# Optimization experiments

Hardware: AMD Instinct MI355X
Metric: run time of the kernel (lower is better)

The kernel has to match this reference:

```python
import jax, jax.numpy as jnp
import numpy as np

B, C_IN, C_OUT, K, L = 8, 512, 512, 5, 4096
RED = 128  # max(int(512*0.25), 4)
STRIDE, PAD, DIL, GROUPS = 1, 2, 1, 1


def setup_inputs() -> dict:
    key = jax.random.key(0)
    ks = jax.random.split(key, 20)

    def n(k, shape, scale=0.05):
        return jax.random.normal(k, shape, jnp.float32) * scale

    inp = {
        "x": jax.random.normal(ks[0], (B, C_IN, L), jnp.float32),
        "weight": n(ks[1], (C_OUT, C_IN // GROUPS, K), 0.05),
        "bias": jnp.zeros((C_OUT,), jnp.float32),
    }
    # four attention branches: avgpool -> 1x1 conv (C_in->RED) -> relu -> 1x1 conv (RED->out) -> sigmoid
    for i, (nm, od) in enumerate(zip(["ka", "sa", "ia", "oa"], [K, 1, C_IN, C_OUT])):
        inp[nm + "_w1"] = n(ks[2 + 4 * i], (RED, C_IN))
        inp[nm + "_b1"] = jnp.zeros((RED,), jnp.float32)
        inp[nm + "_w2"] = n(ks[3 + 4 * i], (od, RED))
        inp[nm + "_b2"] = jnp.zeros((od,), jnp.float32)
    return inp


def _att(avg, w1, b1, w2, b2):
    # avg: [B, C_in]; two 1x1 convs over a length-1 signal == two dense layers
    h = jax.nn.relu(avg @ w1.T + b1)
    return jax.nn.sigmoid(h @ w2.T + b2)


def reference(x, weight, bias,
              ka_w1, ka_b1, ka_w2, ka_b2,
              sa_w1, sa_b1, sa_w2, sa_b2,
              ia_w1, ia_b1, ia_w2, ia_b2,
              oa_w1, oa_b1, oa_w2, oa_b2):
    b, c, l = x.shape
    avg = x.mean(axis=2)                     # AdaptiveAvgPool1d(1) -> [B, C_in]
    ka = _att(avg, ka_w1, ka_b1, ka_w2, ka_b2)  # [B, K]
    sa = _att(avg, sa_w1, sa_b1, sa_w2, sa_b2)  # [B, 1]
    ia = _att(avg, ia_w1, ia_b1, ia_w2, ia_b2)  # [B, C_in]
    oa = _att(avg, oa_w1, oa_b1, oa_w2, oa_b2)  # [B, C_out]
    # dynamic weight [B, C_out, C_in//g, K]; note ia broadcasts on the OUT-channel
    # axis (faithful to the torch broadcasting, which requires C_in == C_out)
    dw = (weight[None]
          * ka[:, None, None, :]
          * sa[:, :, None, None]
          * ia[:, :, None, None]
          * oa[:, :, None, None])
    dw = dw.reshape(b * C_OUT, C_IN // GROUPS, K)
    xg = x.reshape(1, b * c, l)
    out = jax.lax.conv_general_dilated(
        xg, dw,
        window_strides=(STRIDE,),
        padding=[(PAD, PAD)],
        rhs_dilation=(DIL,),
        feature_group_count=b * GROUPS,
        dimension_numbers=("NCH", "OIH", "NCH"))
    out = out.reshape(b, C_OUT, -1) + bias[None, :, None]
    return out
```

## Files before the change

### kernel.cpp

```cpp
#include <hip/hip_runtime.h>

typedef unsigned short u16;
typedef __bf16 bf16x8 __attribute__((ext_vector_type(8)));
typedef float f32x4 __attribute__((ext_vector_type(4)));
typedef u16 u16x8 __attribute__((ext_vector_type(8)));

#define B_    8
#define CIN   512
#define COUT  512
#define KT    5
#define LEN   4096
#define RED_  128
#define KDIM  (KT * CIN)
#define XTROWS (LEN + 4)
#define NLT   64

__device__ __forceinline__ u16 f2bf(float f) {
    unsigned int u = __float_as_uint(f);
    u += 0x7fffu + ((u >> 16) & 1u);
    return (u16)(u >> 16);
}

typedef __attribute__((address_space(1))) void gvoid_t;
typedef __attribute__((address_space(3))) void lvoid_t;
__device__ __forceinline__ void glds16(const u16* g, u16* l) {
    __builtin_amdgcn_global_load_lds((gvoid_t*)g, (lvoid_t*)l, 16, 0, 0);
}

__global__ __launch_bounds__(256) void xtavg_kernel(const float* __restrict__ x,
                                                    u16* __restrict__ xt,
                                                    float* __restrict__ P) {
    __shared__ __align__(16) unsigned Tu[64 * 65];
    __shared__ float Fp[64 * 2 * 17];
    const int b  = blockIdx.z;
    const int l0 = blockIdx.x * 64;
    const int c0 = blockIdx.y * 128;
    const int tid = threadIdx.x;
    const int lq  = tid & 15;
    const int cpg = tid >> 4;

#pragma unroll
    for (int p = 0; p < 4; ++p) {
        const int cp = p * 16 + cpg;
        const int c  = c0 + cp * 2;
        const float* xa = x + ((size_t)b * CIN + c) * LEN + l0 + lq * 4;
        float4 va = *(const float4*)xa;
        float4 vb = *(const float4*)(xa + LEN);
        unsigned u0 = __builtin_amdgcn_perm(__float_as_uint(vb.x), __float_as_uint(va.x), 0x07060302);
        unsigned u1 = __builtin_amdgcn_perm(__float_as_uint(vb.y), __float_as_uint(va.y), 0x07060302);
        unsigned u2 = __builtin_amdgcn_perm(__float_as_uint(vb.z), __float_as_uint(va.z), 0x07060302);
        unsigned u3 = __builtin_amdgcn_perm(__float_as_uint(vb.w), __float_as_uint(va.w), 0x07060302);
        Tu[(lq * 4 + 0) * 65 + cp] = u0;
        Tu[(lq * 4 + 1) * 65 + cp] = u1;
        Tu[(lq * 4 + 2) * 65 + cp] = u2;
        Tu[(lq * 4 + 3) * 65 + cp] = u3;
        Fp[(cp * 2 + 0) * 17 + lq] = va.x + va.y + va.z + va.w;
        Fp[(cp * 2 + 1) * 17 + lq] = vb.x + vb.y + vb.z + vb.w;
    }
    __syncthreads();

#pragma unroll
    for (int p = 0; p < 4; ++p) {
        const int r  = p * 16 + (tid >> 4);
        const int j4 = (tid & 15) * 4;
        unsigned w0 = Tu[r * 65 + j4 + 0];
        unsigned w1 = Tu[r * 65 + j4 + 1];
        unsigned w2 = Tu[r * 65 + j4 + 2];
        unsigned w3 = Tu[r * 65 + j4 + 3];
        *(uint4*)(xt + ((size_t)b * XTROWS + l0 + 2 + r) * CIN + c0 + j4 * 2) =
            make_uint4(w0, w1, w2, w3);
    }
    if (tid < 128) {
        const float* fp = &Fp[tid * 17];
        float s = 0.f;
#pragma unroll
        for (int k = 0; k < 16; ++k) s += fp[k];
        P[(size_t)blockIdx.x * (B_ * CIN) + b * CIN + c0 + tid] = s;
    }
    if (blockIdx.y == 0 && blockIdx.x == 0 && tid < 128)
        *(uint4*)(xt + ((size_t)b * XTROWS + (tid >> 6)) * CIN + (tid & 63) * 8) =
            make_uint4(0, 0, 0, 0);
    if (blockIdx.y == 0 && blockIdx.x == (LEN / 64 - 1) && tid < 128)
        *(uint4*)(xt + ((size_t)b * XTROWS + LEN + 2 + (tid >> 6)) * CIN + (tid & 63) * 8) =
            make_uint4(0, 0, 0, 0);
}

__global__ void attn_kernel(const float* __restrict__ P,
    const float* kw1, const float* kb1, const float* kw2, const float* kb2,
    const float* sw1, const float* sb1, const float* sw2, const float* sb2,
    const float* iw1, const float* ib1, const float* iw2, const float* ib2,
    const float* ow1, const float* ob1, const float* ow2, const float* ob2,
    float* __restrict__ ka, float* __restrict__ sa,
    float* __restrict__ ia, float* __restrict__ oa) {
    const int br = blockIdx.x >> 3, b = blockIdx.x & 7;
    const float *w1, *b1p, *w2, *b2p; float* op; int od;
    if (br == 0)      { w1 = kw1; b1p = kb1; w2 = kw2; b2p = kb2; op = ka + b * KT;  od = KT;   }
    else if (br == 1) { w1 = sw1; b1p = sb1; w2 = sw2; b2p = sb2; op = sa + b;       od = 1;    }
    else if (br == 2) { w1 = iw1; b1p = ib1; w2 = iw2; b2p = ib2; op = ia + b * CIN; od = CIN;  }
    else              { w1 = ow1; b1p = ob1; w2 = ow2; b2p = ob2; op = oa + b * COUT; od = COUT; }

    __shared__ float av[4 * 132];
    __shared__ float h[RED_];
    const int t = threadIdx.x;
    {
        const float* pp = P + b * CIN + t;
        float ssum = 0.f;
#pragma unroll 8
        for (int lt = 0; lt < NLT; ++lt) ssum += pp[(size_t)lt * (B_ * CIN)];
        av[(t >> 7) * 132 + (t & 127)] = ssum * (1.0f / LEN);
    }
    __syncthreads();

    const int row = t >> 2, part = t & 3;
    float acc = 0.f;
    const float4* wr = (const float4*)(w1 + (size_t)row * CIN + part * 128);
    const float* ap = &av[part * 132];
#pragma unroll 8
    for (int c = 0; c < 32; ++c) {
        float4 w = wr[c];
        acc += ap[4 * c] * w.x + ap[4 * c + 1] * w.y + ap[4 * c + 2] * w.z + ap[4 * c + 3] * w.w;
    }
    acc += __shfl_down(acc, 1, 64);
    acc += __shfl_down(acc, 2, 64);
    if (part == 0) h[row] = fmaxf(acc + b1p[row], 0.f);
    __syncthreads();

    for (int o = t; o < od; o += 512) {
        float a2 = b2p[o];
        const float4* w2r = (const float4*)(w2 + (size_t)o * RED_);
#pragma unroll 8
        for (int j = 0; j < RED_ / 4; ++j) {
            float4 w = w2r[j];
            a2 += h[4 * j] * w.x + h[4 * j + 1] * w.y + h[4 * j + 2] * w.z + h[4 * j + 3] * w.w;
        }
        op[o] = 1.f / (1.f + expf(-a2));
    }
}

__global__ void wbgen_kernel(const float* __restrict__ w, const float* __restrict__ ka,
                             u16* __restrict__ wb) {
    __shared__ float kv[B_ * KT];
    const int tid = threadIdx.x;
    if (tid < B_ * KT) kv[tid] = ka[tid];
    __syncthreads();
    const int o  = (blockIdx.x >> 2) * 4 + (tid >> 6);
    const int b0 = (blockIdx.x & 3) * 2;
    const int i8 = (tid & 63) * 8;

    const float* wp = w + ((size_t)o * CIN + i8) * KT;
    float wv[40];
#pragma unroll
    for (int q = 0; q < 10; ++q) {
        float4 v = ((const float4*)wp)[q];
        wv[4 * q] = v.x; wv[4 * q + 1] = v.y; wv[4 * q + 2] = v.z; wv[4 * q + 3] = v.w;
    }
#pragma unroll
    for (int bb = 0; bb < 2; ++bb) {
        const int b = b0 + bb;
#pragma unroll
        for (int k = 0; k < KT; ++k) {
            const float s = kv[b * KT + k];
            u16x8 r;
#pragma unroll
            for (int j = 0; j < 8; ++j) r[j] = f2bf(wv[j * KT + k] * s);
            *(u16x8*)(wb + ((size_t)(b * COUT + o)) * KDIM + k * CIN + i8) = r;
        }
    }
}

__global__ __launch_bounds__(256, 2) void gemm_kernel(
    const u16* __restrict__ wb, const u16* __restrict__ xt,
    const float* __restrict__ sa, const float* __restrict__ ia,
    const float* __restrict__ oa, const float* __restrict__ bias,
    float* __restrict__ out) {
    __shared__ __align__(16) u16 As[5 * 128 * 32];
    __shared__ __align__(16) u16 Bs[260 * 32];
    __shared__ float sm[128], bm[128];

    const int orig = blockIdx.x;
    const int wg   = (orig & 7) * 64 + (orig >> 3);
    const int l0 = (wg & 15) * 256;
    const int o0 = ((wg >> 4) & 3) * 128;
    const int b  = wg >> 6;
    const int tid = threadIdx.x;

    if (tid < 128) {
        sm[tid] = sa[b] * ia[b * CIN + o0 + tid] * oa[b * COUT + o0 + tid];
        bm[tid] = bias[o0 + tid];
    }

    const int lane = tid & 63;
    const int wave = tid >> 6;
    const int wm = (wave >> 1) * 64;
    const int wn = (wave & 1) * 128;
    const int lm = lane & 15;
    const int quad = lane >> 4;

    f32x4 acc[4][8];
#pragma unroll
    for (int i = 0; i < 4; ++i)
#pragma unroll
        for (int j = 0; j < 8; ++j) {
            f32x4 zz = {0.f, 0.f, 0.f, 0.f};
            acc[i][j] = zz;
        }

    const u16* gA = wb + ((size_t)(b * COUT + o0 + (tid >> 2))) * KDIM + (tid & 3) * 8;
    const u16* gB = xt + ((size_t)b * XTROWS + l0) * CIN;

#pragma unroll 1
    for (int ic = 0; ic < 16; ++ic) {
        const int i0 = ic * 32;
#pragma unroll
        for (int t = 0; t < KT; ++t) {
            glds16(gA + t * 512 + i0, &As[t * 4096 + tid * 8]);
            glds16(gA + (size_t)64 * KDIM + t * 512 + i0, &As[t * 4096 + 2048 + tid * 8]);
        }
#pragma unroll
        for (int r = 0; r < 4; ++r) {
            const int slot = r * 256 + tid;
            glds16(gB + (size_t)(slot >> 2) * CIN + i0 + (slot & 3) * 8, &Bs[slot * 8]);
        }
        if (tid < 16)
            glds16(gB + (size_t)(256 + (tid >> 2)) * CIN + i0 + (tid & 3) * 8,
                   &Bs[(1024 + tid) * 8]);
        __syncthreads();

#pragma unroll
        for (int t = 0; t < KT; ++t) {
            bf16x8 af[4], bfr[8];
#pragma unroll
            for (int f = 0; f < 4; ++f)
                af[f] = *(const bf16x8*)&As[t * 4096 + (wm + f * 16 + lm) * 32 + quad * 8];
#pragma unroll
            for (int f = 0; f < 8; ++f)
                bfr[f] = *(const bf16x8*)&Bs[(wn + f * 16 + lm + t) * 32 + quad * 8];
#pragma unroll
            for (int mt = 0; mt < 4; ++mt)
#pragma unroll
                for (int nt = 0; nt < 8; ++nt)
                    acc[mt][nt] = __builtin_amdgcn_mfma_f32_16x16x32_bf16(
                        af[mt], bfr[nt], acc[mt][nt], 0, 0, 0);
        }
        __syncthreads();
    }

#pragma unroll
    for (int mt = 0; mt < 4; ++mt) {
        const int mb = wm + mt * 16 + quad * 4;
        float sv[4], bv[4];
#pragma unroll
        for (int r = 0; r < 4; ++r) { sv[r] = sm[mb + r]; bv[r] = bm[mb + r]; }
#pragma unroll
        for (int nt = 0; nt < 8; ++nt) {
            const int col = l0 + wn + nt * 16 + lm;
            float* op = out + ((size_t)(b * COUT + o0 + mb)) * LEN + col;
#pragma unroll
            for (int r = 0; r < 4; ++r)
                op[(size_t)r * LEN] = sv[r] * acc[mt][nt][r] + bv[r];
        }
    }
}

extern "C" void kernel_launch(void* const* d_in, const int* in_sizes, int n_in,
                              void* d_out, int out_size, void* d_ws, size_t ws_size,
                              hipStream_t stream) {
    const float* x      = (const float*)d_in[0];
    const float* weight = (const float*)d_in[1];
    const float* bias   = (const float*)d_in[2];
    float* out = (float*)d_out;

    char* ws = (char*)d_ws;
    size_t off = 0;
    auto alloc = [&](size_t bytes) {
        void* p = ws + off;
        off += (bytes + 255) & ~(size_t)255;
        return p;
    };
    u16*   wbuf = (u16*)alloc((size_t)B_ * COUT * KDIM * sizeof(u16));
    u16*   xtb  = (u16*)alloc((size_t)B_ * XTROWS * CIN * sizeof(u16));
    float* Pbuf = (float*)alloc((size_t)NLT * B_ * CIN * sizeof(float));
    float* ka   = (float*)alloc((size_t)B_ * KT * sizeof(float));
    float* sa   = (float*)alloc((size_t)B_ * sizeof(float));
    float* ia   = (float*)alloc((size_t)B_ * CIN * sizeof(float));
    float* oa   = (float*)alloc((size_t)B_ * COUT * sizeof(float));

    xtavg_kernel<<<dim3(LEN / 64, CIN / 128, B_), 256, 0, stream>>>(x, xtb, Pbuf);
    attn_kernel<<<32, 512, 0, stream>>>(Pbuf,
        (const float*)d_in[3],  (const float*)d_in[4],  (const float*)d_in[5],  (const float*)d_in[6],
        (const float*)d_in[7],  (const float*)d_in[8],  (const float*)d_in[9],  (const float*)d_in[10],
        (const float*)d_in[11], (const float*)d_in[12], (const float*)d_in[13], (const float*)d_in[14],
        (const float*)d_in[15], (const float*)d_in[16], (const float*)d_in[17], (const float*)d_in[18],
        ka, sa, ia, oa);
    wbgen_kernel<<<(COUT / 4) * 4, 256, 0, stream>>>(weight, ka, wbuf);
    gemm_kernel<<<512, 256, 0, stream>>>(wbuf, xtb, sa, ia, oa, bias, out);
}
```

Before: 241.2 us.

## Fuse attention branches and weight generation into one prep kernel with redundant ka

Merges the attention kernel and the dynamic-weight generation kernel into a single launch. Each of the 1024 weight-gen blocks recomputes the kernel-attention (ka) branch for its batch locally, which removes the dependency on a separate launch. 32 extra blocks are launched and 24 of them compute the sa/ia/oa branches, which are only consumed later by the GEMM. This drops one kernel launch and its serialization gap. In exchange, every weight-gen block redundantly reads the partial sums and the ka weights.

```diff
diff --git a/kernel.cpp b/kernel.cpp
--- a/kernel.cpp
+++ b/kernel.cpp
@@ -85,48 +85,34 @@
             make_uint4(0, 0, 0, 0);
 }
 
-__global__ void attn_kernel(const float* __restrict__ P,
-    const float* kw1, const float* kb1, const float* kw2, const float* kb2,
-    const float* sw1, const float* sb1, const float* sw2, const float* sb2,
-    const float* iw1, const float* ib1, const float* iw2, const float* ib2,
-    const float* ow1, const float* ob1, const float* ow2, const float* ob2,
-    float* __restrict__ ka, float* __restrict__ sa,
-    float* __restrict__ ia, float* __restrict__ oa) {
-    const int br = blockIdx.x >> 3, b = blockIdx.x & 7;
-    const float *w1, *b1p, *w2, *b2p; float* op; int od;
-    if (br == 0)      { w1 = kw1; b1p = kb1; w2 = kw2; b2p = kb2; op = ka + b * KT;  od = KT;   }
-    else if (br == 1) { w1 = sw1; b1p = sb1; w2 = sw2; b2p = sb2; op = sa + b;       od = 1;    }
-    else if (br == 2) { w1 = iw1; b1p = ib1; w2 = iw2; b2p = ib2; op = ia + b * CIN; od = CIN;  }
-    else              { w1 = ow1; b1p = ob1; w2 = ow2; b2p = ob2; op = oa + b * COUT; od = COUT; }
-
-    __shared__ float av[4 * 132];
-    __shared__ float h[RED_];
-    const int t = threadIdx.x;
-    {
-        const float* pp = P + b * CIN + t;
-        float ssum = 0.f;
+__device__ __forceinline__ void attn_branch(
+    int tid, const float* __restrict__ P,
+    const float* w1, const float* b1, const float* w2, const float* b2,
+    float* op, int od, int b, float* av, float* h) {
+#pragma unroll
+    for (int half = 0; half < 2; ++half) {
+        const int ch = tid + half * 256;
+        const float* pp = P + b * CIN + ch;
+        float s = 0.f;
 #pragma unroll 8
-        for (int lt = 0; lt < NLT; ++lt) ssum += pp[(size_t)lt * (B_ * CIN)];
-        av[(t >> 7) * 132 + (t & 127)] = ssum * (1.0f / LEN);
+        for (int lt = 0; lt < NLT; ++lt) s += pp[(size_t)lt * (B_ * CIN)];
+        av[ch] = s * (1.0f / LEN);
     }
     __syncthreads();
-
-    const int row = t >> 2, part = t & 3;
+    const int row = tid >> 1, part = tid & 1;
     float acc = 0.f;
-    const float4* wr = (const float4*)(w1 + (size_t)row * CIN + part * 128);
-    const float* ap = &av[part * 132];
+    const float4* wr = (const float4*)(w1 + (size_t)row * CIN + part * 256);
+    const float* ap = av + part * 256;
 #pragma unroll 8
-    for (int c = 0; c < 32; ++c) {
+    for (int c = 0; c < 64; ++c) {
         float4 w = wr[c];
         acc += ap[4 * c] * w.x + ap[4 * c + 1] * w.y + ap[4 * c + 2] * w.z + ap[4 * c + 3] * w.w;
     }
     acc += __shfl_down(acc, 1, 64);
-    acc += __shfl_down(acc, 2, 64);
-    if (part == 0) h[row] = fmaxf(acc + b1p[row], 0.f);
+    if (part == 0) h[row] = fmaxf(acc + b1[row], 0.f);
     __syncthreads();
-
-    for (int o = t; o < od; o += 512) {
-        float a2 = b2p[o];
+    for (int o = tid; o < od; o += 256) {
+        float a2 = b2[o];
         const float4* w2r = (const float4*)(w2 + (size_t)o * RED_);
 #pragma unroll 8
         for (int j = 0; j < RED_ / 4; ++j) {
@@ -137,34 +123,50 @@
     }
 }
 
-__global__ void wbgen_kernel(const float* __restrict__ w, const float* __restrict__ ka,
-                             u16* __restrict__ wb) {
-    __shared__ float kv[B_ * KT];
+__global__ __launch_bounds__(256) void prep2_kernel(
+    const float* __restrict__ P, const float* __restrict__ weight,
+    const float* kw1, const float* kb1, const float* kw2, const float* kb2,
+    const float* sw1, const float* sb1, const float* sw2, const float* sb2,
+    const float* iw1, const float* ib1, const float* iw2, const float* ib2,
+    const float* ow1, const float* ob1, const float* ow2, const float* ob2,
+    float* __restrict__ sa, float* __restrict__ ia, float* __restrict__ oa,
+    u16* __restrict__ wb) {
+    __shared__ float av[CIN];
+    __shared__ float h[RED_];
+    __shared__ float kv[KT];
     const int tid = threadIdx.x;
-    if (tid < B_ * KT) kv[tid] = ka[tid];
-    __syncthreads();
-    const int o  = (blockIdx.x >> 2) * 4 + (tid >> 6);
-    const int b0 = (blockIdx.x & 3) * 2;
-    const int i8 = (tid & 63) * 8;
-
-    const float* wp = w + ((size_t)o * CIN + i8) * KT;
-    float wv[40];
-#pragma unroll
-    for (int q = 0; q < 10; ++q) {
-        float4 v = ((const float4*)wp)[q];
-        wv[4 * q] = v.x; wv[4 * q + 1] = v.y; wv[4 * q + 2] = v.z; wv[4 * q + 3] = v.w;
-    }
-#pragma unroll
-    for (int bb = 0; bb < 2; ++bb) {
-        const int b = b0 + bb;
+
+    if (blockIdx.x < 1024) {
+        const int og = (int)blockIdx.x >> 3;
+        const int b  = (int)blockIdx.x & 7;
+        attn_branch(tid, P, kw1, kb1, kw2, kb2, kv, KT, b, av, h);
+        __syncthreads();
+        const int o  = og * 4 + (tid >> 6);
+        const int i8 = (tid & 63) * 8;
+        const float* wp = weight + ((size_t)o * CIN + i8) * KT;
+        float wv[40];
+#pragma unroll
+        for (int q = 0; q < 10; ++q) {
+            float4 v = ((const float4*)wp)[q];
+            wv[4 * q] = v.x; wv[4 * q + 1] = v.y; wv[4 * q + 2] = v.z; wv[4 * q + 3] = v.w;
+        }
 #pragma unroll
         for (int k = 0; k < KT; ++k) {
-            const float s = kv[b * KT + k];
+            const float s = kv[k];
             u16x8 r;
 #pragma unroll
             for (int j = 0; j < 8; ++j) r[j] = f2bf(wv[j * KT + k] * s);
             *(u16x8*)(wb + ((size_t)(b * COUT + o)) * KDIM + k * CIN + i8) = r;
         }
+    } else {
+        const int vb = (int)blockIdx.x - 1024;
+        if (vb >= 24) return;
+        const int br = vb >> 3, b = vb & 7;
+        const float *w1, *b1, *w2, *b2; float* op; int od;
+        if (br == 0)      { w1 = sw1; b1 = sb1; w2 = sw2; b2 = sb2; op = sa + b;        od = 1;    }
+        else if (br == 1) { w1 = iw1; b1 = ib1; w2 = iw2; b2 = ib2; op = ia + b * CIN;  od = CIN;  }
+        else              { w1 = ow1; b1 = ob1; w2 = ow2; b2 = ob2; op = oa + b * COUT; od = COUT; }
+        attn_branch(tid, P, w1, b1, w2, b2, op, od, b, av, h);
     }
 }
 
@@ -280,18 +282,16 @@
     u16*   wbuf = (u16*)alloc((size_t)B_ * COUT * KDIM * sizeof(u16));
     u16*   xtb  = (u16*)alloc((size_t)B_ * XTROWS * CIN * sizeof(u16));
     float* Pbuf = (float*)alloc((size_t)NLT * B_ * CIN * sizeof(float));
-    float* ka   = (float*)alloc((size_t)B_ * KT * sizeof(float));
     float* sa   = (float*)alloc((size_t)B_ * sizeof(float));
     float* ia   = (float*)alloc((size_t)B_ * CIN * sizeof(float));
     float* oa   = (float*)alloc((size_t)B_ * COUT * sizeof(float));
 
     xtavg_kernel<<<dim3(LEN / 64, CIN / 128, B_), 256, 0, stream>>>(x, xtb, Pbuf);
-    attn_kernel<<<32, 512, 0, stream>>>(Pbuf,
+    prep2_kernel<<<1056, 256, 0, stream>>>(Pbuf, weight,
         (const float*)d_in[3],  (const float*)d_in[4],  (const float*)d_in[5],  (const float*)d_in[6],
         (const float*)d_in[7],  (const float*)d_in[8],  (const float*)d_in[9],  (const float*)d_in[10],
         (const float*)d_in[11], (const float*)d_in[12], (const float*)d_in[13], (const float*)d_in[14],
         (const float*)d_in[15], (const float*)d_in[16], (const float*)d_in[17], (const float*)d_in[18],
-        ka, sa, ia, oa);
-    wbgen_kernel<<<(COUT / 4) * 4, 256, 0, stream>>>(weight, ka, wbuf);
+        sa, ia, oa, wbuf);
     gemm_kernel<<<512, 256, 0, stream>>>(wbuf, xtb, sa, ia, oa, bias, out);
 }
```

After: 268.9 us. 11.5% more time.

## Double-buffer GEMM LDS tiles and split work across 8 waves per block

Applied to the files above, without the earlier changes.

The GEMM kernel now uses 512 threads with 8 waves, each computing a 64x64 subtile, and double-buffers the A and B LDS tiles. It prefetches the next input-channel chunk via direct global-to-LDS loads while computing the current one, syncing with vmcnt waits and raw barriers. The goal is to hide global load latency behind MFMA work. The trade-offs are doubled LDS use, which limits the kernel to one block per CU, and a lower MFMA-to-LDS-read ratio per wave.

```diff
diff --git a/kernel.cpp b/kernel.cpp
--- a/kernel.cpp
+++ b/kernel.cpp
@@ -168,13 +168,13 @@
     }
 }
 
-__global__ __launch_bounds__(256, 2) void gemm_kernel(
+__global__ __launch_bounds__(512, 2) void gemm_kernel(
     const u16* __restrict__ wb, const u16* __restrict__ xt,
     const float* __restrict__ sa, const float* __restrict__ ia,
     const float* __restrict__ oa, const float* __restrict__ bias,
     float* __restrict__ out) {
-    __shared__ __align__(16) u16 As[5 * 128 * 32];
-    __shared__ __align__(16) u16 Bs[260 * 32];
+    __shared__ __align__(16) u16 As[2][5 * 128 * 32];
+    __shared__ __align__(16) u16 Bs[2][260 * 32];
     __shared__ float sm[128], bm[128];
 
     const int orig = blockIdx.x;
@@ -191,16 +191,16 @@
 
     const int lane = tid & 63;
     const int wave = tid >> 6;
-    const int wm = (wave >> 1) * 64;
-    const int wn = (wave & 1) * 128;
+    const int wm = (wave >> 2) * 64;
+    const int wn = (wave & 3) * 64;
     const int lm = lane & 15;
     const int quad = lane >> 4;
 
-    f32x4 acc[4][8];
+    f32x4 acc[4][4];
 #pragma unroll
     for (int i = 0; i < 4; ++i)
 #pragma unroll
-        for (int j = 0; j < 8; ++j) {
+        for (int j = 0; j < 4; ++j) {
             f32x4 zz = {0.f, 0.f, 0.f, 0.f};
             acc[i][j] = zz;
         }
@@ -208,42 +208,54 @@
     const u16* gA = wb + ((size_t)(b * COUT + o0 + (tid >> 2))) * KDIM + (tid & 3) * 8;
     const u16* gB = xt + ((size_t)b * XTROWS + l0) * CIN;
 
+#define STAGE(B_IDX, IC)                                                            \
+    do {                                                                            \
+        const int i0_ = (IC) * 32;                                                  \
+        _Pragma("unroll")                                                           \
+        for (int t_ = 0; t_ < KT; ++t_)                                             \
+            glds16(gA + t_ * 512 + i0_, &As[B_IDX][t_ * 4096 + tid * 8]);           \
+        _Pragma("unroll")                                                           \
+        for (int r_ = 0; r_ < 2; ++r_) {                                            \
+            const int s_ = r_ * 512 + tid;                                          \
+            glds16(gB + (size_t)(s_ >> 2) * CIN + i0_ + (s_ & 3) * 8,               \
+                   &Bs[B_IDX][s_ * 8]);                                             \
+        }                                                                           \
+        if (tid < 16)                                                               \
+            glds16(gB + (size_t)(256 + (tid >> 2)) * CIN + i0_ + (tid & 3) * 8,     \
+                   &Bs[B_IDX][(1024 + tid) * 8]);                                   \
+    } while (0)
+
+    STAGE(0, 0);
+
 #pragma unroll 1
     for (int ic = 0; ic < 16; ++ic) {
-        const int i0 = ic * 32;
+        const int cur = ic & 1;
+        if (ic < 15) {
+            STAGE(cur ^ 1, ic + 1);
+            asm volatile("s_waitcnt vmcnt(7)" ::: "memory");
+        } else {
+            asm volatile("s_waitcnt vmcnt(0)" ::: "memory");
+        }
+        __builtin_amdgcn_s_barrier();
+
 #pragma unroll
         for (int t = 0; t < KT; ++t) {
-            glds16(gA + t * 512 + i0, &As[t * 4096 + tid * 8]);
-            glds16(gA + (size_t)64 * KDIM + t * 512 + i0, &As[t * 4096 + 2048 + tid * 8]);
-        }
-#pragma unroll
-        for (int r = 0; r < 4; ++r) {
-            const int slot = r * 256 + tid;
-            glds16(gB + (size_t)(slot >> 2) * CIN + i0 + (slot & 3) * 8, &Bs[slot * 8]);
-        }
-        if (tid < 16)
-            glds16(gB + (size_t)(256 + (tid >> 2)) * CIN + i0 + (tid & 3) * 8,
-                   &Bs[(1024 + tid) * 8]);
-        __syncthreads();
-
-#pragma unroll
-        for (int t = 0; t < KT; ++t) {
-            bf16x8 af[4], bfr[8];
-#pragma unroll
-            for (int f = 0; f < 4; ++f)
-                af[f] = *(const bf16x8*)&As[t * 4096 + (wm + f * 16 + lm) * 32 + quad * 8];
-#pragma unroll
-            for (int f = 0; f < 8; ++f)
-                bfr[f] = *(const bf16x8*)&Bs[(wn + f * 16 + lm + t) * 32 + quad * 8];
+            bf16x8 af[4], bfr[4];
+#pragma unroll
+            for (int f = 0; f < 4; ++f) {
+                af[f]  = *(const bf16x8*)&As[cur][t * 4096 + (wm + f * 16 + lm) * 32 + quad * 8];
+                bfr[f] = *(const bf16x8*)&Bs[cur][(wn + f * 16 + lm + t) * 32 + quad * 8];
+            }
 #pragma unroll
             for (int mt = 0; mt < 4; ++mt)
 #pragma unroll
-                for (int nt = 0; nt < 8; ++nt)
+                for (int nt = 0; nt < 4; ++nt)
                     acc[mt][nt] = __builtin_amdgcn_mfma_f32_16x16x32_bf16(
                         af[mt], bfr[nt], acc[mt][nt], 0, 0, 0);
         }
-        __syncthreads();
-    }
+        __builtin_amdgcn_s_barrier();
+    }
+#undef STAGE
 
 #pragma unroll
     for (int mt = 0; mt < 4; ++mt) {
@@ -252,7 +264,7 @@
 #pragma unroll
         for (int r = 0; r < 4; ++r) { sv[r] = sm[mb + r]; bv[r] = bm[mb + r]; }
 #pragma unroll
-        for (int nt = 0; nt < 8; ++nt) {
+        for (int nt = 0; nt < 4; ++nt) {
             const int col = l0 + wn + nt * 16 + lm;
             float* op = out + ((size_t)(b * COUT + o0 + mb)) * LEN + col;
 #pragma unroll
@@ -293,5 +305,5 @@
         (const float*)d_in[15], (const float*)d_in[16], (const float*)d_in[17], (const float*)d_in[18],
         ka, sa, ia, oa);
     wbgen_kernel<<<(COUT / 4) * 4, 256, 0, stream>>>(weight, ka, wbuf);
-    gemm_kernel<<<512, 256, 0, stream>>>(wbuf, xtb, sa, ia, oa, bias, out);
-}
+    gemm_kernel<<<512, 512, 0, stream>>>(wbuf, xtb, sa, ia, oa, bias, out);
+}
```

Measured after the change: 253.2 us. 5.0% more time.
